# Kernel optimization log

Measured on AMD Instinct MI355X. Metric: run time of the kernel, lower is better.

## Reference

```python
import jax, jax.numpy as jnp
import numpy as np

NUM_HEADS = 12
HEAD_CH = 64
WINDOW = 4


def _relative_to_absolute(x):
    # x: (B, H, L, 2L-1) -> (B, H, L, L) via skew trick
    B, H, L, _ = x.shape
    x = jnp.pad(x, ((0, 0), (0, 0), (0, 0), (0, 1)))        # (B,H,L,2L)
    x = x.reshape(B, H, L * 2 * L)
    x = jnp.pad(x, ((0, 0), (0, 0), (0, L - 1)))
    x = x.reshape(B, H, L + 1, 2 * L - 1)
    return x[:, :, :L, L - 1:]


def _get_relative_embeddings(emb, L):
    # emb: (H, 2W+1, D) -> (H, 2L-1, D)
    pad = max(0, L - WINDOW - 1)
    start = max(0, WINDOW - L + 1)
    e = jnp.pad(emb, ((0, 0), (pad, pad), (0, 0)))
    return e[:, start:start + 2 * L - 1, :]


def _forward(x, wq, bq, wk, bk, wv, bv, wo, bo, emb_rel_k, emb_rel_v):
    B, C, L = x.shape
    H, D = NUM_HEADS, HEAD_CH
    scale = 1.0 / np.sqrt(D).astype(np.float32)

    # 1x1 conv == channel matmul
    q = jnp.einsum('oc,bcl->bol', wq, x) + bq[None, :, None]
    k = jnp.einsum('oc,bcl->bol', wk, x) + bk[None, :, None]
    v = jnp.einsum('oc,bcl->bol', wv, x) + bv[None, :, None]

    # (B, C, L) -> (B, H, L, D)
    q = q.reshape(B, H, D, L).transpose(0, 1, 3, 2)
    k = k.reshape(B, H, D, L).transpose(0, 1, 3, 2)
    v = v.reshape(B, H, D, L).transpose(0, 1, 3, 2)

    score = jnp.einsum('bhld,bhmd->bhlm', q, k) * scale      # (B,H,L,L)

    rel_k = _get_relative_embeddings(emb_rel_k, L)           # (H, 2L-1, D)
    s_rel = jnp.einsum('bhld,hmd->bhlm', q, rel_k)           # (B,H,L,2L-1)
    score = score + _relative_to_absolute(s_rel) * scale

    attn = jax.nn.softmax(score, axis=-1)                    # dropout p=0 -> identity

    res = jnp.einsum('bhlm,bhmd->bhld', attn, v)             # (B,H,L,D)

    # absolute_to_relative skew
    a = jnp.pad(attn, ((0, 0), (0, 0), (0, 0), (0, L - 1)))
    a = a.reshape(B, H, L * (2 * L - 1))
    a = jnp.pad(a, ((0, 0), (0, 0), (L, 0)))
    rel_w = a.reshape(B, H, L, 2 * L)[:, :, :, 1:]           # (B,H,L,2L-1)

    rel_v = _get_relative_embeddings(emb_rel_v, L)           # (H, 2L-1, D)
    res = res + jnp.einsum('bhlm,hmd->bhld', rel_w, rel_v)

    res = res.transpose(0, 1, 3, 2).reshape(B, H * D, L)     # (B, C, L)
    out = jnp.einsum('oc,bcl->bol', wo, res) + bo[None, :, None]
    return out


def setup_inputs() -> dict:
    key = jax.random.key(0)
    ks = jax.random.split(key, 11)
    B, C, L = 4, 768, 1024
    rel_std = HEAD_CH ** (-0.5)
    xavier = np.sqrt(6.0 / (C + C)).astype(np.float32)
    return {
        'x': jax.random.normal(ks[0], (B, C, L), jnp.float32),
        'wq': jax.random.uniform(ks[1], (C, C), jnp.float32, -xavier, xavier),
        'bq': jnp.zeros((C,), jnp.float32),
        'wk': jax.random.uniform(ks[2], (C, C), jnp.float32, -xavier, xavier),
        'bk': jnp.zeros((C,), jnp.float32),
        'wv': jax.random.uniform(ks[3], (C, C), jnp.float32, -xavier, xavier),
        'bv': jnp.zeros((C,), jnp.float32),
        'wo': jax.random.normal(ks[4], (C, C), jnp.float32) * 0.02,
        'bo': jnp.zeros((C,), jnp.float32),
        'emb_rel_k': jax.random.normal(ks[5], (NUM_HEADS, 2 * WINDOW + 1, HEAD_CH), jnp.float32) * rel_std,
        'emb_rel_v': jax.random.normal(ks[6], (NUM_HEADS, 2 * WINDOW + 1, HEAD_CH), jnp.float32) * rel_std,
    }


def reference(x, wq, bq, wk, bk, wv, bv, wo, bo, emb_rel_k, emb_rel_v):
    return _forward(x, wq, bq, wk, bk, wv, bv, wo, bo, emb_rel_k, emb_rel_v)
```

## Files before the change

kernel.cpp:

```cpp
#include <hip/hip_runtime.h>

#define NB   4
#define NH   12
#define HD   64
#define CCH  768
#define LQ   1024
#define SCALE 0.125f
#define STAB  4.0f
#define WELE (CCH*CCH)

typedef unsigned short u16;
typedef __bf16 bf16x8 __attribute__((ext_vector_type(8)));
typedef unsigned short u16x8 __attribute__((ext_vector_type(8)));
typedef unsigned short u16x4 __attribute__((ext_vector_type(4)));
typedef float floatx4 __attribute__((ext_vector_type(4)));

__device__ __forceinline__ float bf2f(u16 u) {
    union { unsigned int i; float f; } x; x.i = ((unsigned int)u) << 16; return x.f;
}
__device__ __forceinline__ u16 f2bf_u(float f) {
    union { float f; unsigned int i; } x; x.f = f;
    unsigned int i = x.i;
    return (u16)((i + 0x7FFFu + ((i >> 16) & 1u)) >> 16);
}
__device__ __forceinline__ void glds16(const u16* g, u16* l) {
    __builtin_amdgcn_global_load_lds(
        (const __attribute__((address_space(1))) unsigned int*)g,
        (__attribute__((address_space(3))) unsigned int*)l, 16, 0, 0);
}

__global__ __launch_bounds__(256) void convert_w_kernel(
    const float* __restrict__ wq, const float* __restrict__ wk,
    const float* __restrict__ wv, const float* __restrict__ wo,
    u16* __restrict__ wb)
{
    const int p = blockIdx.y;
    const float* src = (p == 0) ? wq : (p == 1) ? wk : (p == 2) ? wv : wo;
    u16* dst = wb + (size_t)p * WELE;
    const int idx = (blockIdx.x * 256 + threadIdx.x) * 4;
    const float4 v = *reinterpret_cast<const float4*>(src + idx);
    u16x4 o;
    o[0] = f2bf_u(v.x); o[1] = f2bf_u(v.y); o[2] = f2bf_u(v.z); o[3] = f2bf_u(v.w);
    *reinterpret_cast<u16x4*>(dst + idx) = o;
}

__global__ __launch_bounds__(256) void transpose_x_kernel(
    const float* __restrict__ x, u16* __restrict__ xT)
{
    __shared__ u16 tile[64 * 68];
    const int l0 = blockIdx.x * 64, c0 = blockIdx.y * 64, b = blockIdx.z;
    const int t = threadIdx.x;
    const float* xb = x + (size_t)b * CCH * LQ;
    {
        const int l = t & 63, cg = t >> 6;
        for (int i = 0; i < 16; ++i) {
            const int c = cg * 16 + i;
            tile[c * 68 + l] = f2bf_u(xb[(size_t)(c0 + c) * LQ + l0 + l]);
        }
    }
    __syncthreads();
    {
        const int c = t & 63, lg = t >> 6;
        for (int i = 0; i < 16; ++i) {
            const int l = lg * 16 + i;
            xT[((size_t)b * LQ + l0 + l) * CCH + c0 + c] = tile[c * 68 + l];
        }
    }
}

#define GEMM_CORE(Ag, Bg)                                                     \
    __shared__ __align__(16) u16 a_tile[128 * 64];                            \
    __shared__ __align__(16) u16 b_tile[128 * 64];                            \
    const int t = threadIdx.x;                                                \
    const int wave = t >> 6, lane = t & 63;                                   \
    const int quad = lane >> 4, l16 = lane & 15;                              \
    const int wm = (wave >> 1) * 64, wn = (wave & 1) * 64;                    \
    floatx4 acc[4][4];                                                        \
    _Pragma("unroll") for (int mi = 0; mi < 4; ++mi)                          \
        _Pragma("unroll") for (int ni = 0; ni < 4; ++ni)                      \
            _Pragma("unroll") for (int r = 0; r < 4; ++r) acc[mi][ni][r] = 0.f;\
    for (int k0 = 0; k0 < CCH; k0 += 64) {                                    \
        __syncthreads();                                                      \
        _Pragma("unroll") for (int i = 0; i < 4; ++i) {                       \
            const int sbase = wave * 256 + i * 64;                            \
            const int s = sbase + lane;                                       \
            const int m = s >> 3, pos = s & 7;                                \
            const int gpos = pos ^ (m & 7);                                   \
            glds16(Ag + (size_t)(m0 + m) * CCH + k0 + gpos * 8,               \
                   &a_tile[sbase * 8]);                                       \
            glds16(Bg + (size_t)(n0 + m) * CCH + k0 + gpos * 8,               \
                   &b_tile[sbase * 8]);                                       \
        }                                                                     \
        __syncthreads();                                                      \
        bf16x8 af[2][4], bfr[2][4];                                           \
        _Pragma("unroll") for (int s = 0; s < 2; ++s)                         \
            _Pragma("unroll") for (int i = 0; i < 4; ++i) {                   \
                const int am = wm + i * 16 + l16;                             \
                const int bn = wn + i * 16 + l16;                             \
                const int c = s * 4 + quad;                                   \
                af[s][i]  = *reinterpret_cast<const bf16x8*>(                 \
                    &a_tile[(am * 8 + (c ^ (am & 7))) * 8]);                  \
                bfr[s][i] = *reinterpret_cast<const bf16x8*>(                 \
                    &b_tile[(bn * 8 + (c ^ (bn & 7))) * 8]);                  \
            }                                                                 \
        _Pragma("unroll") for (int s = 0; s < 2; ++s)                         \
            _Pragma("unroll") for (int mi = 0; mi < 4; ++mi)                  \
                _Pragma("unroll") for (int ni = 0; ni < 4; ++ni)              \
                    acc[mi][ni] = __builtin_amdgcn_mfma_f32_16x16x32_bf16(    \
                        af[s][mi], bfr[s][ni], acc[mi][ni], 0, 0, 0);         \
    }

__global__ __launch_bounds__(256) void proj_qkv_kernel(
    const u16* __restrict__ xT, const u16* __restrict__ wb,
    const float* __restrict__ bq, const float* __restrict__ bk,
    const float* __restrict__ bv,
    u16* __restrict__ Qw, u16* __restrict__ Kw, u16* __restrict__ Vw)
{
    const int z = blockIdx.z, b = z / 3, p = z % 3;
    const int n0 = blockIdx.x * 128, m0 = blockIdx.y * 128;
    const u16* Ag = wb + (size_t)p * WELE;
    const u16* Bg = xT + (size_t)b * LQ * CCH;
    const float* bias = (p == 0) ? bq : (p == 1) ? bk : bv;
    u16* Y = ((p == 0) ? Qw : (p == 1) ? Kw : Vw) + (size_t)b * CCH * LQ;

    GEMM_CORE(Ag, Bg)

#pragma unroll
    for (int mi = 0; mi < 4; ++mi) {
#pragma unroll
        for (int r = 0; r < 4; ++r) {
            const int o = m0 + wm + mi * 16 + quad * 4 + r;
            const float bb = bias[o];
#pragma unroll
            for (int ni = 0; ni < 4; ++ni) {
                const int l = n0 + wn + ni * 16 + l16;
                Y[(size_t)o * LQ + l] = f2bf_u(acc[mi][ni][r] + bb);
            }
        }
    }
}

__global__ __launch_bounds__(256) void proj_out_kernel(
    const u16* __restrict__ resb, const u16* __restrict__ wb,
    const float* __restrict__ bo, float* __restrict__ out)
{
    const int b = blockIdx.z;
    const int n0 = blockIdx.x * 128, m0 = blockIdx.y * 128;
    const u16* Ag = wb + (size_t)3 * WELE;
    const u16* Bg = resb + (size_t)b * LQ * CCH;
    float* Y = out + (size_t)b * CCH * LQ;

    GEMM_CORE(Ag, Bg)

#pragma unroll
    for (int mi = 0; mi < 4; ++mi) {
#pragma unroll
        for (int r = 0; r < 4; ++r) {
            const int o = m0 + wm + mi * 16 + quad * 4 + r;
            const float bb = bo[o];
#pragma unroll
            for (int ni = 0; ni < 4; ++ni) {
                const int l = n0 + wn + ni * 16 + l16;
                Y[(size_t)o * LQ + l] = acc[mi][ni][r] + bb;
            }
        }
    }
}

#define KSTRIDE 72

__global__ __launch_bounds__(256) void attn_kernel(
    const u16* __restrict__ Qw, const u16* __restrict__ Kw,
    const u16* __restrict__ Vw,
    const float* __restrict__ erk, const float* __restrict__ erv,
    u16* __restrict__ resb)
{
    __shared__ __align__(16) u16 kv_lds[2 * 64 * KSTRIDE];
    __shared__ __align__(16) u16 p_lds[4 * 16 * KSTRIDE];
    __shared__ float bias_lds[64 * 9];
    __shared__ float bandw_lds[64 * 9];
    __shared__ float erk_lds[9 * 64];
    __shared__ float erv_lds[9 * 64];

    u16* k16 = kv_lds;
    u16* v16 = kv_lds + 64 * KSTRIDE;
    u16* kdiag = kv_lds;

    const int t = threadIdx.x;
    const int wave = t >> 6, lane = t & 63;
    const int quad = lane >> 4, l16 = lane & 15;
    const int l0 = blockIdx.x * 64, h = blockIdx.y, b = blockIdx.z;
    const int rbase = wave * 16;
    const size_t base = ((size_t)b * CCH + (size_t)h * HD) * LQ;
    const u16* Qb = Qw + base;
    const u16* Kb = Kw + base;
    const u16* Vb = Vw + base;

    for (int i = t; i < 9 * 64; i += 256) {
        erk_lds[i] = erk[(size_t)h * 9 * 64 + i];
        erv_lds[i] = erv[(size_t)h * 9 * 64 + i];
    }

    bf16x8 qa0, qa1;
    {
        const int lg = l0 + rbase + l16;
        union { u16x8 u; bf16x8 v; } t0, t1;
#pragma unroll
        for (int jj = 0; jj < 8; ++jj) {
            t0.u[jj] = Qb[(size_t)(quad * 8 + jj) * LQ + lg];
            t1.u[jj] = Qb[(size_t)(32 + quad * 8 + jj) * LQ + lg];
        }
        qa0 = t0.v; qa1 = t1.v;
    }
    __syncthreads();

    {
        union { bf16x8 v; u16x8 u; } a0, a1; a0.v = qa0; a1.v = qa1;
        float qf[16];
#pragma unroll
        for (int jj = 0; jj < 8; ++jj) { qf[jj] = bf2f(a0.u[jj]); qf[8 + jj] = bf2f(a1.u[jj]); }
        for (int dl = 0; dl < 9; ++dl) {
            float s = 0.f;
#pragma unroll
            for (int jj = 0; jj < 8; ++jj) {
                s += qf[jj]     * erk_lds[dl * 64 + quad * 8 + jj];
                s += qf[8 + jj] * erk_lds[dl * 64 + 32 + quad * 8 + jj];
            }
            s += __shfl_xor(s, 16, 64);
            s += __shfl_xor(s, 32, 64);
            if (quad == 0) bias_lds[(rbase + l16) * 9 + dl] = s;
        }
    }

    floatx4 O[4];
    float l_acc = 0.f;
#pragma unroll
    for (int i = 0; i < 4; ++i)
#pragma unroll
        for (int r = 0; r < 4; ++r) O[i][r] = 0.f;

    u16* pw = p_lds + wave * 16 * KSTRIDE;
    const int qrow = rbase + l16;
    const int lgq = l0 + qrow;

    for (int kb = 0; kb < 16; ++kb) {
        const int j0 = kb * 64;
        __syncthreads();
        {
            u16 tmp[16];
#pragma unroll
            for (int dd = 0; dd < 16; ++dd)
                tmp[dd] = Kb[(size_t)(wave * 16 + dd) * LQ + j0 + lane];
            *reinterpret_cast<u16x8*>(&k16[lane * KSTRIDE + wave * 16])     = *reinterpret_cast<u16x8*>(tmp);
            *reinterpret_cast<u16x8*>(&k16[lane * KSTRIDE + wave * 16 + 8]) = *reinterpret_cast<u16x8*>(tmp + 8);
        }
        {
            const int d = t >> 2, seg = t & 3;
            const u16x8* src = reinterpret_cast<const u16x8*>(Vb + (size_t)d * LQ + j0 + seg * 16);
            *reinterpret_cast<u16x8*>(&v16[d * KSTRIDE + seg * 16])     = src[0];
            *reinterpret_cast<u16x8*>(&v16[d * KSTRIDE + seg * 16 + 8]) = src[1];
        }
        __syncthreads();

        floatx4 s4[4];
#pragma unroll
        for (int tt = 0; tt < 4; ++tt) {
            const bf16x8 ka0 = *reinterpret_cast<const bf16x8*>(&k16[(tt * 16 + l16) * KSTRIDE + quad * 8]);
            const bf16x8 ka1 = *reinterpret_cast<const bf16x8*>(&k16[(tt * 16 + l16) * KSTRIDE + 32 + quad * 8]);
            floatx4 c;
#pragma unroll
            for (int r = 0; r < 4; ++r) c[r] = 0.f;
            c = __builtin_amdgcn_mfma_f32_16x16x32_bf16(ka0, qa0, c, 0, 0, 0);
            c = __builtin_amdgcn_mfma_f32_16x16x32_bf16(ka1, qa1, c, 0, 0, 0);
            s4[tt] = c;
        }

        {
            const int lgmin = l0 + rbase, lgmax = lgmin + 15;
            if (j0 + 63 >= lgmin - 4 && j0 <= lgmax + 4) {
#pragma unroll
                for (int tt = 0; tt < 4; ++tt) {
#pragma unroll
                    for (int r = 0; r < 4; ++r) {
                        const int key = j0 + tt * 16 + quad * 4 + r;
                        const int delta = key - lgq + 4;
                        if (delta >= 0 && delta <= 8) s4[tt][r] += bias_lds[qrow * 9 + delta];
                    }
                }
            }
        }

#pragma unroll
        for (int tt = 0; tt < 4; ++tt) {
            u16x4 pk;
#pragma unroll
            for (int r = 0; r < 4; ++r) {
                const float p = __expf(fmaf(s4[tt][r], SCALE, -STAB));
                l_acc += p;
                pk[r] = f2bf_u(p);
            }
            *reinterpret_cast<u16x4*>(&pw[l16 * KSTRIDE + tt * 16 + quad * 4]) = pk;
        }

        const bf16x8 pa0 = *reinterpret_cast<const bf16x8*>(&pw[l16 * KSTRIDE + quad * 8]);
        const bf16x8 pa1 = *reinterpret_cast<const bf16x8*>(&pw[l16 * KSTRIDE + 32 + quad * 8]);
#pragma unroll
        for (int tt = 0; tt < 4; ++tt) {
            const bf16x8 vb0 = *reinterpret_cast<const bf16x8*>(&v16[(tt * 16 + l16) * KSTRIDE + quad * 8]);
            const bf16x8 vb1 = *reinterpret_cast<const bf16x8*>(&v16[(tt * 16 + l16) * KSTRIDE + 32 + quad * 8]);
            O[tt] = __builtin_amdgcn_mfma_f32_16x16x32_bf16(pa0, vb0, O[tt], 0, 0, 0);
            O[tt] = __builtin_amdgcn_mfma_f32_16x16x32_bf16(pa1, vb1, O[tt], 0, 0, 0);
        }
    }

    float l_tot = l_acc;
    l_tot += __shfl_xor(l_tot, 16, 64);
    l_tot += __shfl_xor(l_tot, 32, 64);

    __syncthreads();

    {
#pragma unroll
        for (int dd = 0; dd < 16; ++dd) {
            const int d = wave * 16 + dd;
            int j = l0 - 4 + lane;
            int jc = min(max(j, 0), LQ - 1);
            kdiag[lane * KSTRIDE + d] = Kb[(size_t)d * LQ + jc];
            if (lane < 8) {
                j = l0 + 60 + lane;
                jc = min(j, LQ - 1);
                kdiag[(64 + lane) * KSTRIDE + d] = Kb[(size_t)d * LQ + jc];
            }
        }
    }
    __syncthreads();

    {
        union { bf16x8 v; u16x8 u; } a0, a1; a0.v = qa0; a1.v = qa1;
        float qf[16];
#pragma unroll
        for (int jj = 0; jj < 8; ++jj) { qf[jj] = bf2f(a0.u[jj]); qf[8 + jj] = bf2f(a1.u[jj]); }
        for (int dl = 0; dl < 9; ++dl) {
            union { bf16x8 v; u16x8 u; } k0, k1;
            k0.v = *reinterpret_cast<const bf16x8*>(&kdiag[(qrow + dl) * KSTRIDE + quad * 8]);
            k1.v = *reinterpret_cast<const bf16x8*>(&kdiag[(qrow + dl) * KSTRIDE + 32 + quad * 8]);
            float s = 0.f;
#pragma unroll
            for (int jj = 0; jj < 8; ++jj) {
                s += qf[jj]     * bf2f(k0.u[jj]);
                s += qf[8 + jj] * bf2f(k1.u[jj]);
            }
            s += __shfl_xor(s, 16, 64);
            s += __shfl_xor(s, 32, 64);
            const int jgl = lgq + dl - 4;
            float pband = 0.f;
            if (jgl >= 0 && jgl < LQ)
                pband = __expf(fmaf(s + bias_lds[qrow * 9 + dl], SCALE, -STAB));
            if (quad == 0) bandw_lds[qrow * 9 + dl] = pband;
        }
    }

    float rinv[4];
#pragma unroll
    for (int r = 0; r < 4; ++r) {
        const int src = (lane & 48) | (quad * 4 + r);
        rinv[r] = 1.0f / __shfl(l_tot, src, 64);
    }

#pragma unroll
    for (int tt = 0; tt < 4; ++tt) {
#pragma unroll
        for (int r = 0; r < 4; ++r) {
            const int row = rbase + quad * 4 + r;
            const int d = tt * 16 + l16;
            float val = O[tt][r];
#pragma unroll
            for (int dl = 0; dl < 9; ++dl)
                val += bandw_lds[row * 9 + dl] * erv_lds[dl * 64 + d];
            val *= rinv[r];
            resb[((size_t)b * LQ + (l0 + row)) * CCH + h * HD + d] = f2bf_u(val);
        }
    }
}

extern "C" void kernel_launch(void* const* d_in, const int* in_sizes, int n_in,
                              void* d_out, int out_size, void* d_ws, size_t ws_size,
                              hipStream_t stream) {
    const float* x   = (const float*)d_in[0];
    const float* wq  = (const float*)d_in[1];
    const float* bq  = (const float*)d_in[2];
    const float* wk  = (const float*)d_in[3];
    const float* bk  = (const float*)d_in[4];
    const float* wv  = (const float*)d_in[5];
    const float* bv  = (const float*)d_in[6];
    const float* wo  = (const float*)d_in[7];
    const float* bo  = (const float*)d_in[8];
    const float* erk = (const float*)d_in[9];
    const float* erv = (const float*)d_in[10];
    float* out = (float*)d_out;

    const size_t NEL = (size_t)NB * CCH * LQ;
    u16* xT   = (u16*)d_ws;
    u16* wb   = xT + NEL;
    u16* Qw   = wb + (size_t)4 * WELE;
    u16* Kw   = Qw + NEL;
    u16* Vw   = Kw + NEL;
    u16* resb = Vw + NEL;

    convert_w_kernel<<<dim3(WELE / 1024, 4), 256, 0, stream>>>(wq, wk, wv, wo, wb);
    transpose_x_kernel<<<dim3(16, 12, 4), 256, 0, stream>>>(x, xT);
    proj_qkv_kernel<<<dim3(8, 6, 12), 256, 0, stream>>>(
        xT, wb, bq, bk, bv, Qw, Kw, Vw);
    attn_kernel<<<dim3(LQ / 64, NH, NB), 256, 0, stream>>>(
        Qw, Kw, Vw, erk, erv, resb);
    proj_out_kernel<<<dim3(8, 6, 4), 256, 0, stream>>>(resb, wb, bo, out);
}
```

Measured before the change: 193.5 us.

## Store Q/K row-major and switch attention to 32x32 MFMA with key split

Q and K projections now write in (L, C) layout by swapping GEMM operands, so attention can load Q rows and K tiles with contiguous 16-byte reads instead of strided scalar gathers. The attention kernel moves from 16x16x32 to 32x32x16 MFMA: each wave handles 32 query rows against half of each 64-key block, and the two key halves are merged at the end through LDS. The V projection is split into its own kernel so it keeps the old layout. This costs an extra launch, an LDS reduction step and an extra barrier, and only half the waves do the epilogue.

```diff
diff --git a/kernel.cpp b/kernel.cpp
--- a/kernel.cpp
+++ b/kernel.cpp
@@ -14,6 +14,7 @@
 typedef unsigned short u16x8 __attribute__((ext_vector_type(8)));
 typedef unsigned short u16x4 __attribute__((ext_vector_type(4)));
 typedef float floatx4 __attribute__((ext_vector_type(4)));
+typedef float floatx16 __attribute__((ext_vector_type(16)));
 
 __device__ __forceinline__ float bf2f(u16 u) {
     union { unsigned int i; float f; } x; x.i = ((unsigned int)u) << 16; return x.f;
@@ -110,18 +111,43 @@
                         af[s][mi], bfr[s][ni], acc[mi][ni], 0, 0, 0);         \
     }
 
-__global__ __launch_bounds__(256) void proj_qkv_kernel(
+__global__ __launch_bounds__(256) void proj_qk_kernel(
     const u16* __restrict__ xT, const u16* __restrict__ wb,
     const float* __restrict__ bq, const float* __restrict__ bk,
-    const float* __restrict__ bv,
-    u16* __restrict__ Qw, u16* __restrict__ Kw, u16* __restrict__ Vw)
-{
-    const int z = blockIdx.z, b = z / 3, p = z % 3;
+    u16* __restrict__ Qlc, u16* __restrict__ Klc)
+{
+    const int z = blockIdx.z, b = z >> 1, p = z & 1;
     const int n0 = blockIdx.x * 128, m0 = blockIdx.y * 128;
-    const u16* Ag = wb + (size_t)p * WELE;
+    const u16* Ag = xT + (size_t)b * LQ * CCH;
+    const u16* Bg = wb + (size_t)p * WELE;
+    const float* bias = (p == 0) ? bq : bk;
+    u16* Y = ((p == 0) ? Qlc : Klc) + (size_t)b * LQ * CCH;
+
+    GEMM_CORE(Ag, Bg)
+
+#pragma unroll
+    for (int ni = 0; ni < 4; ++ni) {
+        const int o = n0 + wn + ni * 16 + l16;
+        const float bb = bias[o];
+#pragma unroll
+        for (int mi = 0; mi < 4; ++mi)
+#pragma unroll
+            for (int r = 0; r < 4; ++r) {
+                const int l = m0 + wm + mi * 16 + quad * 4 + r;
+                Y[(size_t)l * CCH + o] = f2bf_u(acc[mi][ni][r] + bb);
+            }
+    }
+}
+
+__global__ __launch_bounds__(256) void proj_v_kernel(
+    const u16* __restrict__ xT, const u16* __restrict__ wb,
+    const float* __restrict__ bv, u16* __restrict__ Vw)
+{
+    const int b = blockIdx.z;
+    const int n0 = blockIdx.x * 128, m0 = blockIdx.y * 128;
+    const u16* Ag = wb + (size_t)2 * WELE;
     const u16* Bg = xT + (size_t)b * LQ * CCH;
-    const float* bias = (p == 0) ? bq : (p == 1) ? bk : bv;
-    u16* Y = ((p == 0) ? Qw : (p == 1) ? Kw : Vw) + (size_t)b * CCH * LQ;
+    u16* Y = Vw + (size_t)b * CCH * LQ;
 
     GEMM_CORE(Ag, Bg)
 
@@ -130,7 +156,7 @@
 #pragma unroll
         for (int r = 0; r < 4; ++r) {
             const int o = m0 + wm + mi * 16 + quad * 4 + r;
-            const float bb = bias[o];
+            const float bb = bv[o];
 #pragma unroll
             for (int ni = 0; ni < 4; ++ni) {
                 const int l = n0 + wn + ni * 16 + l16;
@@ -168,217 +194,222 @@
 }
 
 #define KSTRIDE 72
-
-__global__ __launch_bounds__(256) void attn_kernel(
-    const u16* __restrict__ Qw, const u16* __restrict__ Kw,
+#define PSTR 40
+
+__global__ __launch_bounds__(256, 4) void attn_kernel(
+    const u16* __restrict__ Qlc, const u16* __restrict__ Klc,
     const u16* __restrict__ Vw,
     const float* __restrict__ erk, const float* __restrict__ erv,
     u16* __restrict__ resb)
 {
     __shared__ __align__(16) u16 kv_lds[2 * 64 * KSTRIDE];
-    __shared__ __align__(16) u16 p_lds[4 * 16 * KSTRIDE];
+    __shared__ __align__(16) u16 p_lds[4 * 32 * PSTR];
     __shared__ float bias_lds[64 * 9];
     __shared__ float bandw_lds[64 * 9];
     __shared__ float erk_lds[9 * 64];
     __shared__ float erv_lds[9 * 64];
+    __shared__ float l_red[64];
 
     u16* k16 = kv_lds;
     u16* v16 = kv_lds + 64 * KSTRIDE;
+    float* ored = (float*)kv_lds;
     u16* kdiag = kv_lds;
 
     const int t = threadIdx.x;
     const int wave = t >> 6, lane = t & 63;
-    const int quad = lane >> 4, l16 = lane & 15;
+    const int hw = lane >> 5, l32 = lane & 31;
+    const int qh = wave & 1, kh = wave >> 1;
     const int l0 = blockIdx.x * 64, h = blockIdx.y, b = blockIdx.z;
-    const int rbase = wave * 16;
-    const size_t base = ((size_t)b * CCH + (size_t)h * HD) * LQ;
-    const u16* Qb = Qw + base;
-    const u16* Kb = Kw + base;
-    const u16* Vb = Vw + base;
+
+    const u16* Qb = Qlc + (size_t)b * LQ * CCH + h * HD;
+    const u16* Kb = Klc + (size_t)b * LQ * CCH + h * HD;
+    const u16* Vb = Vw + ((size_t)b * CCH + h * HD) * LQ;
 
     for (int i = t; i < 9 * 64; i += 256) {
         erk_lds[i] = erk[(size_t)h * 9 * 64 + i];
         erv_lds[i] = erv[(size_t)h * 9 * 64 + i];
     }
 
-    bf16x8 qa0, qa1;
-    {
-        const int lg = l0 + rbase + l16;
-        union { u16x8 u; bf16x8 v; } t0, t1;
-#pragma unroll
-        for (int jj = 0; jj < 8; ++jj) {
-            t0.u[jj] = Qb[(size_t)(quad * 8 + jj) * LQ + lg];
-            t1.u[jj] = Qb[(size_t)(32 + quad * 8 + jj) * LQ + lg];
-        }
-        qa0 = t0.v; qa1 = t1.v;
-    }
-    __syncthreads();
-
-    {
-        union { bf16x8 v; u16x8 u; } a0, a1; a0.v = qa0; a1.v = qa1;
-        float qf[16];
-#pragma unroll
-        for (int jj = 0; jj < 8; ++jj) { qf[jj] = bf2f(a0.u[jj]); qf[8 + jj] = bf2f(a1.u[jj]); }
+    const int qrow = qh * 32 + l32;
+    const int lgq = l0 + qrow;
+
+    bf16x8 qa[4];
+#pragma unroll
+    for (int c = 0; c < 4; ++c)
+        qa[c] = *reinterpret_cast<const bf16x8*>(&Qb[(size_t)lgq * CCH + c * 16 + hw * 8]);
+
+    __syncthreads();
+
+    if (kh == 0) {
+        float qf[32];
+#pragma unroll
+        for (int c = 0; c < 4; ++c) {
+            union { bf16x8 v; u16x8 u; } a; a.v = qa[c];
+#pragma unroll
+            for (int j = 0; j < 8; ++j) qf[c * 8 + j] = bf2f(a.u[j]);
+        }
         for (int dl = 0; dl < 9; ++dl) {
             float s = 0.f;
 #pragma unroll
-            for (int jj = 0; jj < 8; ++jj) {
-                s += qf[jj]     * erk_lds[dl * 64 + quad * 8 + jj];
-                s += qf[8 + jj] * erk_lds[dl * 64 + 32 + quad * 8 + jj];
-            }
-            s += __shfl_xor(s, 16, 64);
+            for (int c = 0; c < 4; ++c)
+#pragma unroll
+                for (int j = 0; j < 8; ++j)
+                    s += qf[c * 8 + j] * erk_lds[dl * 64 + c * 16 + hw * 8 + j];
             s += __shfl_xor(s, 32, 64);
-            if (quad == 0) bias_lds[(rbase + l16) * 9 + dl] = s;
-        }
-    }
-
-    floatx4 O[4];
+            if (hw == 0) bias_lds[qrow * 9 + dl] = s;
+        }
+    }
+
+    floatx16 O[2];
+#pragma unroll
+    for (int dt = 0; dt < 2; ++dt)
+#pragma unroll
+        for (int r = 0; r < 16; ++r) O[dt][r] = 0.f;
     float l_acc = 0.f;
-#pragma unroll
-    for (int i = 0; i < 4; ++i)
-#pragma unroll
-        for (int r = 0; r < 4; ++r) O[i][r] = 0.f;
-
-    u16* pw = p_lds + wave * 16 * KSTRIDE;
-    const int qrow = rbase + l16;
-    const int lgq = l0 + qrow;
+
+    u16* pw = p_lds + wave * 32 * PSTR;
 
     for (int kb = 0; kb < 16; ++kb) {
         const int j0 = kb * 64;
         __syncthreads();
         {
-            u16 tmp[16];
-#pragma unroll
-            for (int dd = 0; dd < 16; ++dd)
-                tmp[dd] = Kb[(size_t)(wave * 16 + dd) * LQ + j0 + lane];
-            *reinterpret_cast<u16x8*>(&k16[lane * KSTRIDE + wave * 16])     = *reinterpret_cast<u16x8*>(tmp);
-            *reinterpret_cast<u16x8*>(&k16[lane * KSTRIDE + wave * 16 + 8]) = *reinterpret_cast<u16x8*>(tmp + 8);
-        }
-        {
-            const int d = t >> 2, seg = t & 3;
-            const u16x8* src = reinterpret_cast<const u16x8*>(Vb + (size_t)d * LQ + j0 + seg * 16);
-            *reinterpret_cast<u16x8*>(&v16[d * KSTRIDE + seg * 16])     = src[0];
-            *reinterpret_cast<u16x8*>(&v16[d * KSTRIDE + seg * 16 + 8]) = src[1];
+            const int j = t >> 2, seg = t & 3;
+            const u16x8* ks = reinterpret_cast<const u16x8*>(&Kb[(size_t)(j0 + j) * CCH + seg * 16]);
+            *reinterpret_cast<u16x8*>(&k16[j * KSTRIDE + seg * 16])     = ks[0];
+            *reinterpret_cast<u16x8*>(&k16[j * KSTRIDE + seg * 16 + 8]) = ks[1];
+            const u16x8* vs = reinterpret_cast<const u16x8*>(&Vb[(size_t)j * LQ + j0 + seg * 16]);
+            *reinterpret_cast<u16x8*>(&v16[j * KSTRIDE + seg * 16])     = vs[0];
+            *reinterpret_cast<u16x8*>(&v16[j * KSTRIDE + seg * 16 + 8]) = vs[1];
         }
         __syncthreads();
 
-        floatx4 s4[4];
-#pragma unroll
-        for (int tt = 0; tt < 4; ++tt) {
-            const bf16x8 ka0 = *reinterpret_cast<const bf16x8*>(&k16[(tt * 16 + l16) * KSTRIDE + quad * 8]);
-            const bf16x8 ka1 = *reinterpret_cast<const bf16x8*>(&k16[(tt * 16 + l16) * KSTRIDE + 32 + quad * 8]);
-            floatx4 c;
-#pragma unroll
-            for (int r = 0; r < 4; ++r) c[r] = 0.f;
-            c = __builtin_amdgcn_mfma_f32_16x16x32_bf16(ka0, qa0, c, 0, 0, 0);
-            c = __builtin_amdgcn_mfma_f32_16x16x32_bf16(ka1, qa1, c, 0, 0, 0);
-            s4[tt] = c;
-        }
-
-        {
-            const int lgmin = l0 + rbase, lgmax = lgmin + 15;
-            if (j0 + 63 >= lgmin - 4 && j0 <= lgmax + 4) {
-#pragma unroll
-                for (int tt = 0; tt < 4; ++tt) {
-#pragma unroll
-                    for (int r = 0; r < 4; ++r) {
-                        const int key = j0 + tt * 16 + quad * 4 + r;
-                        const int delta = key - lgq + 4;
-                        if (delta >= 0 && delta <= 8) s4[tt][r] += bias_lds[qrow * 9 + delta];
-                    }
-                }
-            }
-        }
-
-#pragma unroll
-        for (int tt = 0; tt < 4; ++tt) {
-            u16x4 pk;
-#pragma unroll
-            for (int r = 0; r < 4; ++r) {
-                const float p = __expf(fmaf(s4[tt][r], SCALE, -STAB));
-                l_acc += p;
-                pk[r] = f2bf_u(p);
-            }
-            *reinterpret_cast<u16x4*>(&pw[l16 * KSTRIDE + tt * 16 + quad * 4]) = pk;
-        }
-
-        const bf16x8 pa0 = *reinterpret_cast<const bf16x8*>(&pw[l16 * KSTRIDE + quad * 8]);
-        const bf16x8 pa1 = *reinterpret_cast<const bf16x8*>(&pw[l16 * KSTRIDE + 32 + quad * 8]);
-#pragma unroll
-        for (int tt = 0; tt < 4; ++tt) {
-            const bf16x8 vb0 = *reinterpret_cast<const bf16x8*>(&v16[(tt * 16 + l16) * KSTRIDE + quad * 8]);
-            const bf16x8 vb1 = *reinterpret_cast<const bf16x8*>(&v16[(tt * 16 + l16) * KSTRIDE + 32 + quad * 8]);
-            O[tt] = __builtin_amdgcn_mfma_f32_16x16x32_bf16(pa0, vb0, O[tt], 0, 0, 0);
-            O[tt] = __builtin_amdgcn_mfma_f32_16x16x32_bf16(pa1, vb1, O[tt], 0, 0, 0);
-        }
-    }
-
-    float l_tot = l_acc;
-    l_tot += __shfl_xor(l_tot, 16, 64);
-    l_tot += __shfl_xor(l_tot, 32, 64);
-
+        floatx16 sc;
+#pragma unroll
+        for (int r = 0; r < 16; ++r) sc[r] = 0.f;
+#pragma unroll
+        for (int c = 0; c < 4; ++c) {
+            const bf16x8 ka = *reinterpret_cast<const bf16x8*>(
+                &k16[(kh * 32 + l32) * KSTRIDE + c * 16 + hw * 8]);
+            sc = __builtin_amdgcn_mfma_f32_32x32x16_bf16(ka, qa[c], sc, 0, 0, 0);
+        }
+
+        const int kbase = j0 + kh * 32;
+        if (kbase + 31 >= l0 + qh * 32 - 4 && kbase <= l0 + qh * 32 + 35) {
+#pragma unroll
+            for (int r = 0; r < 16; ++r) {
+                const int key = kbase + (r & 3) + 8 * (r >> 2) + 4 * hw;
+                const int delta = key - lgq + 4;
+                if (delta >= 0 && delta <= 8) sc[r] += bias_lds[qrow * 9 + delta];
+            }
+        }
+
+        u16 pk[16];
+#pragma unroll
+        for (int r = 0; r < 16; ++r) {
+            const float p = __expf(fmaf(sc[r], SCALE, -STAB));
+            l_acc += p;
+            pk[r] = f2bf_u(p);
+        }
+#pragma unroll
+        for (int g = 0; g < 4; ++g)
+            *reinterpret_cast<u16x4*>(&pw[l32 * PSTR + 8 * g + 4 * hw]) =
+                *reinterpret_cast<const u16x4*>(&pk[4 * g]);
+
+#pragma unroll
+        for (int c2 = 0; c2 < 2; ++c2) {
+            const bf16x8 pa = *reinterpret_cast<const bf16x8*>(
+                &pw[l32 * PSTR + c2 * 16 + hw * 8]);
+#pragma unroll
+            for (int dt = 0; dt < 2; ++dt) {
+                const bf16x8 vb = *reinterpret_cast<const bf16x8*>(
+                    &v16[(dt * 32 + l32) * KSTRIDE + kh * 32 + c2 * 16 + hw * 8]);
+                O[dt] = __builtin_amdgcn_mfma_f32_32x32x16_bf16(pa, vb, O[dt], 0, 0, 0);
+            }
+        }
+    }
+
+    l_acc += __shfl_xor(l_acc, 32, 64);
+
+    __syncthreads();
+    if (kh == 1) {
+        if (hw == 0) l_red[qrow] = l_acc;
+#pragma unroll
+        for (int dt = 0; dt < 2; ++dt)
+#pragma unroll
+            for (int r = 0; r < 16; ++r) {
+                const int row = (r & 3) + 8 * (r >> 2) + 4 * hw;
+                ored[(qh * 32 + row) * 64 + dt * 32 + l32] = O[dt][r];
+            }
+    }
+    __syncthreads();
+    if (kh == 0) {
+        const float linv = 1.0f / (l_acc + l_red[qrow]);
+#pragma unroll
+        for (int dt = 0; dt < 2; ++dt)
+#pragma unroll
+            for (int r = 0; r < 16; ++r) {
+                const int row = (r & 3) + 8 * (r >> 2) + 4 * hw;
+                O[dt][r] += ored[(qh * 32 + row) * 64 + dt * 32 + l32];
+            }
+        if (hw == 0) l_red[qrow] = linv;
+    }
     __syncthreads();
 
     {
-#pragma unroll
-        for (int dd = 0; dd < 16; ++dd) {
-            const int d = wave * 16 + dd;
-            int j = l0 - 4 + lane;
-            int jc = min(max(j, 0), LQ - 1);
-            kdiag[lane * KSTRIDE + d] = Kb[(size_t)d * LQ + jc];
-            if (lane < 8) {
-                j = l0 + 60 + lane;
-                jc = min(j, LQ - 1);
-                kdiag[(64 + lane) * KSTRIDE + d] = Kb[(size_t)d * LQ + jc];
-            }
-        }
-    }
-    __syncthreads();
-
-    {
-        union { bf16x8 v; u16x8 u; } a0, a1; a0.v = qa0; a1.v = qa1;
-        float qf[16];
-#pragma unroll
-        for (int jj = 0; jj < 8; ++jj) { qf[jj] = bf2f(a0.u[jj]); qf[8 + jj] = bf2f(a1.u[jj]); }
+        const int i0 = t >> 2, seg = t & 3;
+        const int jc = min(max(l0 - 4 + i0, 0), LQ - 1);
+        const u16x8* s0 = reinterpret_cast<const u16x8*>(&Kb[(size_t)jc * CCH + seg * 16]);
+        *reinterpret_cast<u16x8*>(&kdiag[i0 * KSTRIDE + seg * 16])     = s0[0];
+        *reinterpret_cast<u16x8*>(&kdiag[i0 * KSTRIDE + seg * 16 + 8]) = s0[1];
+        if (t < 32) {
+            const int i1 = 64 + (t >> 2);
+            const int j2 = min(l0 - 4 + i1, LQ - 1);
+            const u16x8* s1 = reinterpret_cast<const u16x8*>(&Kb[(size_t)j2 * CCH + seg * 16]);
+            *reinterpret_cast<u16x8*>(&kdiag[i1 * KSTRIDE + seg * 16])     = s1[0];
+            *reinterpret_cast<u16x8*>(&kdiag[i1 * KSTRIDE + seg * 16 + 8]) = s1[1];
+        }
+    }
+    __syncthreads();
+
+    if (kh == 0) {
+        float qf[32];
+#pragma unroll
+        for (int c = 0; c < 4; ++c) {
+            union { bf16x8 v; u16x8 u; } a; a.v = qa[c];
+#pragma unroll
+            for (int j = 0; j < 8; ++j) qf[c * 8 + j] = bf2f(a.u[j]);
+        }
         for (int dl = 0; dl < 9; ++dl) {
-            union { bf16x8 v; u16x8 u; } k0, k1;
-            k0.v = *reinterpret_cast<const bf16x8*>(&kdiag[(qrow + dl) * KSTRIDE + quad * 8]);
-            k1.v = *reinterpret_cast<const bf16x8*>(&kdiag[(qrow + dl) * KSTRIDE + 32 + quad * 8]);
+            const int i = qrow + dl;
             float s = 0.f;
 #pragma unroll
-            for (int jj = 0; jj < 8; ++jj) {
-                s += qf[jj]     * bf2f(k0.u[jj]);
-                s += qf[8 + jj] * bf2f(k1.u[jj]);
-            }
-            s += __shfl_xor(s, 16, 64);
+            for (int c = 0; c < 4; ++c) {
+                union { bf16x8 v; u16x8 u; } kd;
+                kd.v = *reinterpret_cast<const bf16x8*>(&kdiag[i * KSTRIDE + c * 16 + hw * 8]);
+#pragma unroll
+                for (int j = 0; j < 8; ++j) s += qf[c * 8 + j] * bf2f(kd.u[j]);
+            }
             s += __shfl_xor(s, 32, 64);
             const int jgl = lgq + dl - 4;
             float pband = 0.f;
             if (jgl >= 0 && jgl < LQ)
                 pband = __expf(fmaf(s + bias_lds[qrow * 9 + dl], SCALE, -STAB));
-            if (quad == 0) bandw_lds[qrow * 9 + dl] = pband;
-        }
-    }
-
-    float rinv[4];
-#pragma unroll
-    for (int r = 0; r < 4; ++r) {
-        const int src = (lane & 48) | (quad * 4 + r);
-        rinv[r] = 1.0f / __shfl(l_tot, src, 64);
-    }
-
-#pragma unroll
-    for (int tt = 0; tt < 4; ++tt) {
-#pragma unroll
-        for (int r = 0; r < 4; ++r) {
-            const int row = rbase + quad * 4 + r;
-            const int d = tt * 16 + l16;
-            float val = O[tt][r];
-#pragma unroll
-            for (int dl = 0; dl < 9; ++dl)
-                val += bandw_lds[row * 9 + dl] * erv_lds[dl * 64 + d];
-            val *= rinv[r];
-            resb[((size_t)b * LQ + (l0 + row)) * CCH + h * HD + d] = f2bf_u(val);
+            if (hw == 0) bandw_lds[qrow * 9 + dl] = pband;
+        }
+
+#pragma unroll
+        for (int dt = 0; dt < 2; ++dt) {
+#pragma unroll
+            for (int r = 0; r < 16; ++r) {
+                const int row = (r & 3) + 8 * (r >> 2) + 4 * hw;
+                const int d = dt * 32 + l32;
+                float val = O[dt][r];
+#pragma unroll
+                for (int dl = 0; dl < 9; ++dl)
+                    val += bandw_lds[(qh * 32 + row) * 9 + dl] * erv_lds[dl * 64 + d];
+                val *= l_red[qh * 32 + row];
+                resb[((size_t)b * LQ + l0 + qh * 32 + row) * CCH + h * HD + d] = f2bf_u(val);
+            }
         }
     }
 }
@@ -402,16 +433,16 @@
     const size_t NEL = (size_t)NB * CCH * LQ;
     u16* xT   = (u16*)d_ws;
     u16* wb   = xT + NEL;
-    u16* Qw   = wb + (size_t)4 * WELE;
-    u16* Kw   = Qw + NEL;
-    u16* Vw   = Kw + NEL;
+    u16* Qlc  = wb + (size_t)4 * WELE;
+    u16* Klc  = Qlc + NEL;
+    u16* Vw   = Klc + NEL;
     u16* resb = Vw + NEL;
 
     convert_w_kernel<<<dim3(WELE / 1024, 4), 256, 0, stream>>>(wq, wk, wv, wo, wb);
     transpose_x_kernel<<<dim3(16, 12, 4), 256, 0, stream>>>(x, xT);
-    proj_qkv_kernel<<<dim3(8, 6, 12), 256, 0, stream>>>(
-        xT, wb, bq, bk, bv, Qw, Kw, Vw);
+    proj_qk_kernel<<<dim3(6, 8, 8), 256, 0, stream>>>(xT, wb, bq, bk, Qlc, Klc);
+    proj_v_kernel<<<dim3(8, 6, 4), 256, 0, stream>>>(xT, wb, bv, Vw);
     attn_kernel<<<dim3(LQ / 64, NH, NB), 256, 0, stream>>>(
-        Qw, Kw, Vw, erk, erv, resb);
+        Qlc, Klc, Vw, erk, erv, resb);
     proj_out_kernel<<<dim3(8, 6, 4), 256, 0, stream>>>(resb, wb, bo, out);
 }
```

New measurement: 214.6 us. 10.9% more time.
